# Kernel tuning notes

Measured on AMD Instinct MI355X. Metric: run time of the kernel, lower is better.

## Reference

```python
import jax, jax.numpy as jnp
import numpy as np

EMBED = 1024
HEADS = 16
HEAD_DIM = EMBED // HEADS
B, S = 4, 2048


def setup_inputs() -> dict:
    key = jax.random.key(0)
    ks = jax.random.split(key, 13)
    scale = 1.0 / np.sqrt(EMBED)
    inp = {
        "query": jax.random.normal(ks[0], (B, S, EMBED), dtype=jnp.float32),
        "key": jax.random.normal(ks[1], (B, S, EMBED), dtype=jnp.float32),
        "value": jax.random.normal(ks[2], (B, S, EMBED), dtype=jnp.float32),
        "mask": jax.random.randint(ks[3], (B, 1, S, S), 0, 2) > 0,
        "Wq": jax.random.normal(ks[4], (EMBED, EMBED), dtype=jnp.float32) * scale,
        "bq": jnp.zeros((EMBED,), dtype=jnp.float32),
        "Wk": jax.random.normal(ks[5], (EMBED, EMBED), dtype=jnp.float32) * scale,
        "bk": jnp.zeros((EMBED,), dtype=jnp.float32),
        "Wv": jax.random.normal(ks[6], (EMBED, EMBED), dtype=jnp.float32) * scale,
        "bv": jnp.zeros((EMBED,), dtype=jnp.float32),
        "Wo": jax.random.normal(ks[7], (EMBED, EMBED), dtype=jnp.float32) * scale,
        "bo": jnp.zeros((EMBED,), dtype=jnp.float32),
    }
    return inp


def _split_heads(x):
    b, s, _ = x.shape
    return x.reshape(b, s, HEADS, HEAD_DIM).transpose(0, 2, 1, 3)  # [B,H,S,Dh]


def reference(query, key, value, mask, Wq, bq, Wk, bk, Wv, bv, Wo, bo):
    # Linear projections (torch Linear: x @ W.T + b)
    q = _split_heads(query @ Wq.T + bq)
    k = _split_heads(key @ Wk.T + bk)
    v = _split_heads(value @ Wv.T + bv)
    # scaled dot-product attention with full score matrix (as in source)
    scores = jnp.einsum("bhqd,bhkd->bhqk", q, k) / jnp.sqrt(jnp.float32(HEAD_DIM))
    scores = jnp.where(mask, jnp.float32(-1e9), scores)
    attn = jax.nn.softmax(scores, axis=-1)  # dropout p=0 -> identity
    out = jnp.einsum("bhqk,bhkd->bhqd", attn, v)
    out = out.transpose(0, 2, 1, 3).reshape(out.shape[0], -1, EMBED)
    return out @ Wo.T + bo
```

## Files before the change

kernel.cpp:

```cpp
#include <hip/hip_runtime.h>
#include <cstdint>

#define B_  4
#define H_  16
#define S_  2048
#define DH_ 64
#define E_  1024
#define M_  (B_ * S_)

typedef __attribute__((ext_vector_type(8))) __bf16 bf16x8;
typedef __attribute__((ext_vector_type(4))) __bf16 bf16x4;
typedef __attribute__((ext_vector_type(4))) float  f32x4;

__device__ __forceinline__ uint16_t f2bf(float f) {
    union { float f; uint32_t u; } v; v.f = f;
    uint32_t u = v.u;
    uint32_t r = (u + 0x7fffu + ((u >> 16) & 1u)) >> 16;
    return (uint16_t)r;
}
__device__ __forceinline__ uint32_t pack2(float a, float b) {
    return (uint32_t)f2bf(a) | ((uint32_t)f2bf(b) << 16);
}

__device__ __forceinline__ uint32_t cvt_pk_bf16(float lo, float hi) {
    uint32_t r;
    asm("v_cvt_pk_bf16_f32 %0, %1, %2" : "=v"(r) : "v"(lo), "v"(hi));
    return r;
}

__device__ __forceinline__ float exp2_fast(float x) {
#if __has_builtin(__builtin_amdgcn_exp2f)
    return __builtin_amdgcn_exp2f(x);
#else
    float r; asm("v_exp_f32 %0, %1" : "=v"(r) : "v"(x)); return r;
#endif
}

__device__ __forceinline__ void glds16(const void* g, void* lds_base) {
    __builtin_amdgcn_global_load_lds(
        (const __attribute__((address_space(1))) uint32_t*)g,
        (__attribute__((address_space(3))) uint32_t*)lds_base, 16, 0, 0);
}

__global__ void prep_kernel(const float* __restrict__ q, const float* __restrict__ k,
                            const float* __restrict__ v,
                            const float* __restrict__ w0, const float* __restrict__ w1,
                            const float* __restrict__ w2, const float* __restrict__ w3,
                            uint16_t* __restrict__ wbf,
                            uint16_t* __restrict__ qa, uint16_t* __restrict__ ka,
                            uint16_t* __restrict__ va) {
    int bid = blockIdx.x;
    const float* src; uint16_t* dst; int base;
    if (bid < 2048) {
        int i = bid * 256 + threadIdx.x;
        base = i * 8;
        int wsel = base >> 20;
        src = (wsel == 0) ? w0 : (wsel == 1) ? w1 : (wsel == 2) ? w2 : w3;
        dst = wbf + base;
        base &= 1048575;
    } else {
        int r = bid - 2048;
        int sel = r >> 12;
        int i = (r & 4095) * 256 + threadIdx.x;
        base = i * 8;
        src = (sel == 0) ? q : (sel == 1) ? k : v;
        dst = ((sel == 0) ? qa : (sel == 1) ? ka : va) + base;
    }
    float4 a = *(const float4*)(src + base);
    float4 b = *(const float4*)(src + base + 4);
    uint4 o;
    o.x = pack2(a.x, a.y); o.y = pack2(a.z, a.w);
    o.z = pack2(b.x, b.y); o.w = pack2(b.z, b.w);
    *(uint4*)dst = o;
}

__global__ void mask_bits_kernel(const int* __restrict__ mask, uint64_t* __restrict__ bits) {
    int idx = blockIdx.x * 256 + threadIdx.x;
    uint64_t b = __ballot(mask[idx] != 0);
    if ((threadIdx.x & 63) == 0) bits[idx >> 6] = b;
}

__global__ __launch_bounds__(256, 2)
void gemm_bt_kernel(const uint16_t* __restrict__ A0, const uint16_t* __restrict__ A1,
                    const uint16_t* __restrict__ A2,
                    const uint16_t* __restrict__ Bw0,
                    const float* __restrict__ bias0, const float* __restrict__ bias1,
                    const float* __restrict__ bias2,
                    void* __restrict__ out0, void* __restrict__ out1,
                    void* __restrict__ out2,
                    int multi) {
    const int z = blockIdx.z;
    const uint16_t* A  = (z == 0) ? A0 : (z == 1) ? A1 : A2;
    const uint16_t* Bw = Bw0 + (size_t)z * 1048576;
    const float* bias  = (z == 0) ? bias0 : (z == 1) ? bias1 : bias2;
    void* out          = (z == 0) ? out0 : (z == 1) ? out1 : out2;
    const float scale  = (multi && z == 0) ? 0.18033688f : 1.0f;
    const int mode     = multi ? ((z == 2) ? 2 : 1) : 0;

    const int m0 = blockIdx.y * 128;
    const int n0 = blockIdx.x * 128;

    __shared__ __align__(16) uint16_t As[128 * 64];
    __shared__ __align__(16) uint16_t Bs[128 * 64];

    const int t    = threadIdx.x;
    const int w    = t >> 6;
    const int lane = t & 63;
    const int ln   = lane & 15;
    const int quad = lane >> 4;
    const int wr   = w >> 1;
    const int wc   = w & 1;

    f32x4 acc[4][4];
    const f32x4 z4 = {0.f, 0.f, 0.f, 0.f};
#pragma unroll
    for (int i = 0; i < 4; ++i)
#pragma unroll
        for (int j = 0; j < 4; ++j) acc[i][j] = z4;

    const char* Ag = (const char*)(A  + (size_t)m0 * E_);
    const char* Bg = (const char*)(Bw + (size_t)n0 * E_);
    const int rsub = lane >> 3;
    const int colb = ((lane & 7) ^ rsub) * 16;

    for (int kk = 0; kk < E_; kk += 64) {
#pragma unroll
        for (int c = 0; c < 4; ++c) {
            glds16(Ag + (size_t)(c * 32 + w * 8 + rsub) * 2048 + kk * 2 + colb,
                   (char*)As + c * 4096 + w * 1024);
            glds16(Bg + (size_t)(c * 32 + w * 8 + rsub) * 2048 + kk * 2 + colb,
                   (char*)Bs + c * 4096 + w * 1024);
        }
        __syncthreads();

#pragma unroll
        for (int ks = 0; ks < 2; ++ks) {
            bf16x8 af[4], bf[4];
#pragma unroll
            for (int mt = 0; mt < 4; ++mt)
                af[mt] = *(const bf16x8*)&As[(wr * 64 + mt * 16 + ln) * 64 +
                                             (((ks * 4 + quad) ^ (ln & 7)) * 8)];
#pragma unroll
            for (int nt = 0; nt < 4; ++nt)
                bf[nt] = *(const bf16x8*)&Bs[(wc * 64 + nt * 16 + ln) * 64 +
                                             (((ks * 4 + quad) ^ (ln & 7)) * 8)];
#pragma unroll
            for (int mt = 0; mt < 4; ++mt)
#pragma unroll
                for (int nt = 0; nt < 4; ++nt)
                    acc[mt][nt] = __builtin_amdgcn_mfma_f32_16x16x32_bf16(
                        af[mt], bf[nt], acc[mt][nt], 0, 0, 0);
        }
        __syncthreads();
    }

#pragma unroll
    for (int mt = 0; mt < 4; ++mt) {
        const int rowb = m0 + wr * 64 + mt * 16 + quad * 4;
#pragma unroll
        for (int nt = 0; nt < 4; ++nt) {
            const int col = n0 + wc * 64 + nt * 16 + ln;
            const float bsum = bias[col];
            if (mode == 2) {
                int bb = rowb >> 11, s0 = rowb & 2047, hh = col >> 6, d = col & 63;
                float v0 = acc[mt][nt][0] + bsum, v1 = acc[mt][nt][1] + bsum;
                float v2 = acc[mt][nt][2] + bsum, v3 = acc[mt][nt][3] + bsum;
                uint2 o; o.x = pack2(v0, v1); o.y = pack2(v2, v3);
                *(uint2*)((uint16_t*)out + (((size_t)bb * H_ + hh) * DH_ + d) * S_ + s0) = o;
            } else {
#pragma unroll
                for (int r = 0; r < 4; ++r) {
                    float vv = (acc[mt][nt][r] + bsum) * scale;
                    int rr = rowb + r;
                    if (mode == 1) {
                        int bb = rr >> 11, s = rr & 2047, hh = col >> 6, d = col & 63;
                        ((uint16_t*)out)[(((size_t)bb * H_ + hh) * S_ + s) * DH_ + d] = f2bf(vv);
                    } else {
                        ((float*)out)[(size_t)rr * E_ + col] = vv;
                    }
                }
            }
        }
    }
}

__global__ __launch_bounds__(256, 2)
void attn_kernel(const uint16_t* __restrict__ qb, const uint16_t* __restrict__ kb,
                 const uint16_t* __restrict__ vtb, const uint32_t* __restrict__ mbits,
                 uint16_t* __restrict__ attn_out) {
    const int qt = blockIdx.x;
    const int bh = blockIdx.y;
    const int b  = bh >> 4, h = bh & 15;

    __shared__ __align__(16) char smem[51200];
    uint16_t* k_lds  = (uint16_t*)smem;
    uint16_t* vt_lds = (uint16_t*)(smem + 16384);
    uint16_t* p_all  = (uint16_t*)(smem + 32768);
    uint16_t* q_lds  = p_all;

    const int t    = threadIdx.x;
    const int w    = t >> 6;
    const int lane = t & 63;
    const int ln   = lane & 15;
    const int quad = lane >> 4;
    const int ln2  = ln << 1;

    const char* qg  = (const char*)(qb  + ((size_t)bh * S_ + qt * 64) * DH_);
    const char* kg  = (const char*)(kb  + (size_t)bh * S_ * DH_);
    const char* vtg = (const char*)(vtb + (size_t)bh * DH_ * S_);

    glds16(qg + w * 2048 +    0 + lane * 16, (char*)q_lds + w * 2048);
    glds16(qg + w * 2048 + 1024 + lane * 16, (char*)q_lds + w * 2048 + 1024);
    __syncthreads();

    bf16x8 aq[4][2];
#pragma unroll
    for (int mt = 0; mt < 4; ++mt)
#pragma unroll
        for (int ks = 0; ks < 2; ++ks)
            aq[mt][ks] = *(const bf16x8*)&q_lds[(mt * 16 + ln) * 64 + ks * 32 + quad * 8];

    f32x4 acc_o[4][4];
    const f32x4 z4 = {0.f, 0.f, 0.f, 0.f};
#pragma unroll
    for (int mt = 0; mt < 4; ++mt)
#pragma unroll
        for (int nt = 0; nt < 4; ++nt) acc_o[mt][nt] = z4;
    float lr[4][4];
#pragma unroll
    for (int mt = 0; mt < 4; ++mt)
#pragma unroll
        for (int r = 0; r < 4; ++r) lr[mt][r] = 0.f;

    uint16_t* pw = p_all + w * 2304;
    const uint32_t* mwp = mbits + ((size_t)b * S_ + qt * 64) * (S_ / 32);

    for (int it = 0; it < 16; ++it) {
        const char* kt = kg + it * 16384;
        const int rsub = lane >> 3;
        const int kcol = ((lane & 7) ^ rsub) * 16;
#pragma unroll
        for (int c = 0; c < 4; ++c) {
            const int p    = c * 8 + rsub;
            const int jrow = (p < 16) ? (2 * p) : (2 * p - 31);
            glds16(kt + (size_t)(w * 32 + jrow) * 128 + kcol,
                   (char*)k_lds + w * 4096 + c * 1024);
        }
#pragma unroll
        for (int c = 0; c < 4; ++c) {
            int d0  = w * 16 + c * 4;
            int row = d0 + (lane >> 4);
            int gch = (lane & 15) ^ (row & 15);
            glds16(vtg + (size_t)row * (S_ * 2) + it * 256 + gch * 16,
                   (char*)vt_lds + d0 * 256);
        }
        uint32_t mk[4][4];
#pragma unroll
        for (int mt = 0; mt < 4; ++mt)
#pragma unroll
            for (int r = 0; r < 4; ++r)
                mk[mt][r] = mwp[(size_t)(mt * 16 + quad * 4 + r) * 64 + it * 4 + w];
        __syncthreads();

        f32x4 sc[4][2];
#pragma unroll
        for (int mt = 0; mt < 4; ++mt) { sc[mt][0] = z4; sc[mt][1] = z4; }
#pragma unroll
        for (int ks = 0; ks < 2; ++ks) {
            bf16x8 bk0 = *(const bf16x8*)&k_lds[(w * 32 + ln) * 64 +
                                                (((ks * 4 + quad) ^ (ln & 7)) * 8)];
            bf16x8 bk1 = *(const bf16x8*)&k_lds[(w * 32 + 16 + ln) * 64 +
                                                (((ks * 4 + quad) ^ (ln & 7)) * 8)];
#pragma unroll
            for (int mt = 0; mt < 4; ++mt) {
                sc[mt][0] = __builtin_amdgcn_mfma_f32_16x16x32_bf16(aq[mt][ks], bk0, sc[mt][0], 0, 0, 0);
                sc[mt][1] = __builtin_amdgcn_mfma_f32_16x16x32_bf16(aq[mt][ks], bk1, sc[mt][1], 0, 0, 0);
            }
        }

        bf16x8 bv[4];
#pragma unroll
        for (int nt = 0; nt < 4; ++nt)
            bv[nt] = *(const bf16x8*)&vt_lds[(nt * 16 + ln) * 128 +
                                             (((w * 4 + quad) ^ ln) * 8)];

#pragma unroll
        for (int mt = 0; mt < 4; ++mt)
#pragma unroll
            for (int r = 0; r < 4; ++r) {
                uint32_t sh = mk[mt][r] >> ln2;
                float e0 = (sh & 1u) ? 0.f : exp2_fast(sc[mt][0][r]);
                float e1 = (sh & 2u) ? 0.f : exp2_fast(sc[mt][1][r]);
                lr[mt][r] += e0 + e1;
                *(uint32_t*)&pw[(mt * 16 + quad * 4 + r) * 36 + ln2] = cvt_pk_bf16(e0, e1);
            }

#pragma unroll
        for (int mt = 0; mt < 4; ++mt) {
            bf16x4 lo = *(const bf16x4*)&pw[(mt * 16 + ln) * 36 + quad * 8];
            bf16x4 hi = *(const bf16x4*)&pw[(mt * 16 + ln) * 36 + quad * 8 + 4];
            bf16x8 ap = __builtin_shufflevector(lo, hi, 0, 1, 2, 3, 4, 5, 6, 7);
#pragma unroll
            for (int nt = 0; nt < 4; ++nt)
                acc_o[mt][nt] = __builtin_amdgcn_mfma_f32_16x16x32_bf16(ap, bv[nt], acc_o[mt][nt], 0, 0, 0);
        }
        __syncthreads();
    }

#pragma unroll
    for (int mt = 0; mt < 4; ++mt)
#pragma unroll
        for (int r = 0; r < 4; ++r) {
            float v = lr[mt][r];
            v += __shfl_xor(v, 1);
            v += __shfl_xor(v, 2);
            v += __shfl_xor(v, 4);
            v += __shfl_xor(v, 8);
            lr[mt][r] = v;
        }

    __syncthreads();
    float* obuf = (float*)smem;
    float* lbuf = (float*)(smem + 49920);

    if (ln == 0) {
#pragma unroll
        for (int mt = 0; mt < 4; ++mt)
#pragma unroll
            for (int r = 0; r < 4; ++r)
                lbuf[w * 64 + mt * 16 + quad * 4 + r] = lr[mt][r];
    }
#pragma unroll
    for (int mt = 0; mt < 4; ++mt) {
        if (mt != w) {
            int ridx = mt * 3 + (w > mt ? w - 1 : w);
            float* reg = obuf + ridx * 1040;
#pragma unroll
            for (int nt = 0; nt < 4; ++nt)
#pragma unroll
                for (int rr = 0; rr < 4; ++rr)
                    reg[(quad * 4 + rr) * 65 + nt * 16 + ln] = acc_o[mt][nt][rr];
        }
    }
    __syncthreads();

    f32x4 accf[4];
#pragma unroll
    for (int nt = 0; nt < 4; ++nt) accf[nt] = acc_o[0][nt];
#pragma unroll
    for (int mt = 1; mt < 4; ++mt)
        if (w == mt) {
#pragma unroll
            for (int nt = 0; nt < 4; ++nt) accf[nt] = acc_o[mt][nt];
        }
#pragma unroll
    for (int widx = 0; widx < 3; ++widx) {
        const float* reg = obuf + (w * 3 + widx) * 1040;
#pragma unroll
        for (int nt = 0; nt < 4; ++nt)
#pragma unroll
            for (int rr = 0; rr < 4; ++rr)
                accf[nt][rr] += reg[(quad * 4 + rr) * 65 + nt * 16 + ln];
    }
    float invl[4];
#pragma unroll
    for (int rr = 0; rr < 4; ++rr) {
        int row = w * 16 + quad * 4 + rr;
        float lt = lbuf[row] + lbuf[64 + row] + lbuf[128 + row] + lbuf[192 + row];
        invl[rr] = 1.0f / lt;
    }
    const size_t orow = (size_t)(b * S_ + qt * 64 + w * 16 + quad * 4);
#pragma unroll
    for (int rr = 0; rr < 4; ++rr)
#pragma unroll
        for (int nt = 0; nt < 4; ++nt)
            attn_out[(orow + rr) * E_ + h * 64 + nt * 16 + ln] = f2bf(accf[nt][rr] * invl[rr]);
}

extern "C" void kernel_launch(void* const* d_in, const int* in_sizes, int n_in,
                              void* d_out, int out_size, void* d_ws, size_t ws_size,
                              hipStream_t stream) {
    const float* query = (const float*)d_in[0];
    const float* key_  = (const float*)d_in[1];
    const float* value = (const float*)d_in[2];
    const int*   mask  = (const int*)d_in[3];
    const float* Wq = (const float*)d_in[4];
    const float* bq = (const float*)d_in[5];
    const float* Wk = (const float*)d_in[6];
    const float* bk = (const float*)d_in[7];
    const float* Wv = (const float*)d_in[8];
    const float* bv = (const float*)d_in[9];
    const float* Wo = (const float*)d_in[10];
    const float* bo = (const float*)d_in[11];

    char* ws = (char*)d_ws;
    uint16_t* wbf   = (uint16_t*)ws;
    uint16_t* qa    = (uint16_t*)(ws + (8u   << 20));
    uint16_t* ka    = (uint16_t*)(ws + (24u  << 20));
    uint16_t* va    = (uint16_t*)(ws + (40u  << 20));
    uint16_t* qproj = (uint16_t*)(ws + (56u  << 20));
    uint16_t* kproj = (uint16_t*)(ws + (72u  << 20));
    uint16_t* vtp   = (uint16_t*)(ws + (88u  << 20));
    uint16_t* atto  = (uint16_t*)(ws + (104u << 20));
    uint64_t* mbits = (uint64_t*)(ws + (120u << 20));

    prep_kernel<<<14336, 256, 0, stream>>>(query, key_, value, Wq, Wk, Wv, Wo,
                                           wbf, qa, ka, va);
    mask_bits_kernel<<<65536, 256, 0, stream>>>(mask, mbits);

    gemm_bt_kernel<<<dim3(E_ / 128, M_ / 128, 3), 256, 0, stream>>>(
        qa, ka, va, wbf, bq, bk, bv, qproj, kproj, vtp, 1);

    attn_kernel<<<dim3(S_ / 64, B_ * H_), 256, 0, stream>>>(
        qproj, kproj, vtp, (const uint32_t*)mbits, atto);

    gemm_bt_kernel<<<dim3(E_ / 128, M_ / 128, 1), 256, 0, stream>>>(
        atto, atto, atto, wbf + 3145728, bo, bo, bo, d_out, d_out, d_out, 0);
}
```

Before: 456.6 us.

## Load K/V directly into registers with prefetch and remap blocks per XCD

The attention kernel stops staging Q, K and V^T tiles through LDS. Each lane now loads its MFMA fragments straight from global memory, and the next K tile is prefetched into registers one iteration ahead. This removes the per-iteration __syncthreads barriers and the LDS copies. Separately, the grid is flattened to 1D and blocks are remapped so that all query tiles of one batch-head land on the same XCD, which should improve L2 reuse of K/V. The trade-offs are less-coalesced, cache-dependent global loads, higher register pressure, and a prefetch on the last iteration that reads past the end of the current head's K.

```diff
diff --git a/kernel.cpp b/kernel.cpp
--- a/kernel.cpp
+++ b/kernel.cpp
@@ -188,15 +188,15 @@
 void attn_kernel(const uint16_t* __restrict__ qb, const uint16_t* __restrict__ kb,
                  const uint16_t* __restrict__ vtb, const uint32_t* __restrict__ mbits,
                  uint16_t* __restrict__ attn_out) {
-    const int qt = blockIdx.x;
-    const int bh = blockIdx.y;
-    const int b  = bh >> 4, h = bh & 15;
+    const int wg   = blockIdx.x;
+    const int xcd  = wg & 7;
+    const int rest = wg >> 3;
+    const int qt   = rest & 31;
+    const int bh   = ((rest >> 5) << 3) | xcd;
+    const int b    = bh >> 4, h = bh & 15;
 
     __shared__ __align__(16) char smem[51200];
-    uint16_t* k_lds  = (uint16_t*)smem;
-    uint16_t* vt_lds = (uint16_t*)(smem + 16384);
-    uint16_t* p_all  = (uint16_t*)(smem + 32768);
-    uint16_t* q_lds  = p_all;
+    uint16_t* p_all = (uint16_t*)smem;
 
     const int t    = threadIdx.x;
     const int w    = t >> 6;
@@ -209,16 +209,13 @@
     const char* kg  = (const char*)(kb  + (size_t)bh * S_ * DH_);
     const char* vtg = (const char*)(vtb + (size_t)bh * DH_ * S_);
 
-    glds16(qg + w * 2048 +    0 + lane * 16, (char*)q_lds + w * 2048);
-    glds16(qg + w * 2048 + 1024 + lane * 16, (char*)q_lds + w * 2048 + 1024);
-    __syncthreads();
-
     bf16x8 aq[4][2];
 #pragma unroll
     for (int mt = 0; mt < 4; ++mt)
 #pragma unroll
         for (int ks = 0; ks < 2; ++ks)
-            aq[mt][ks] = *(const bf16x8*)&q_lds[(mt * 16 + ln) * 64 + ks * 32 + quad * 8];
+            aq[mt][ks] = *(const bf16x8*)(qg + (size_t)(mt * 16 + ln) * 128 +
+                                          ks * 64 + quad * 16);
 
     f32x4 acc_o[4][4];
     const f32x4 z4 = {0.f, 0.f, 0.f, 0.f};
@@ -233,56 +230,48 @@
         for (int r = 0; r < 4; ++r) lr[mt][r] = 0.f;
 
     uint16_t* pw = p_all + w * 2304;
-    const uint32_t* mwp = mbits + ((size_t)b * S_ + qt * 64) * (S_ / 32);
+
+    const char* kp0 = kg + (size_t)(w * 32 + ln2) * 128 + quad * 16;
+    const char* kp1 = kg + (size_t)(w * 32 + ln2 + 1) * 128 + quad * 16;
+    const char* vp  = vtg + (size_t)ln * 4096 + w * 64 + quad * 16;
+    const char* mp  = (const char*)(mbits + ((size_t)b * S_ + qt * 64) * 64) +
+                      (quad * 4) * 256 + w * 4;
+
+    bf16x8 kf[2][2];
+#pragma unroll
+    for (int ks = 0; ks < 2; ++ks) {
+        kf[ks][0] = *(const bf16x8*)(kp0 + ks * 64);
+        kf[ks][1] = *(const bf16x8*)(kp1 + ks * 64);
+    }
 
     for (int it = 0; it < 16; ++it) {
-        const char* kt = kg + it * 16384;
-        const int rsub = lane >> 3;
-        const int kcol = ((lane & 7) ^ rsub) * 16;
-#pragma unroll
-        for (int c = 0; c < 4; ++c) {
-            const int p    = c * 8 + rsub;
-            const int jrow = (p < 16) ? (2 * p) : (2 * p - 31);
-            glds16(kt + (size_t)(w * 32 + jrow) * 128 + kcol,
-                   (char*)k_lds + w * 4096 + c * 1024);
-        }
-#pragma unroll
-        for (int c = 0; c < 4; ++c) {
-            int d0  = w * 16 + c * 4;
-            int row = d0 + (lane >> 4);
-            int gch = (lane & 15) ^ (row & 15);
-            glds16(vtg + (size_t)row * (S_ * 2) + it * 256 + gch * 16,
-                   (char*)vt_lds + d0 * 256);
-        }
+        bf16x8 bv[4];
+#pragma unroll
+        for (int nt = 0; nt < 4; ++nt)
+            bv[nt] = *(const bf16x8*)(vp + (size_t)nt * 65536);
         uint32_t mk[4][4];
 #pragma unroll
         for (int mt = 0; mt < 4; ++mt)
 #pragma unroll
             for (int r = 0; r < 4; ++r)
-                mk[mt][r] = mwp[(size_t)(mt * 16 + quad * 4 + r) * 64 + it * 4 + w];
-        __syncthreads();
+                mk[mt][r] = *(const uint32_t*)(mp + mt * 4096 + r * 256);
+        bf16x8 kn[2][2];
+#pragma unroll
+        for (int ks = 0; ks < 2; ++ks) {
+            kn[ks][0] = *(const bf16x8*)(kp0 + 16384 + ks * 64);
+            kn[ks][1] = *(const bf16x8*)(kp1 + 16384 + ks * 64);
+        }
 
         f32x4 sc[4][2];
 #pragma unroll
         for (int mt = 0; mt < 4; ++mt) { sc[mt][0] = z4; sc[mt][1] = z4; }
 #pragma unroll
-        for (int ks = 0; ks < 2; ++ks) {
-            bf16x8 bk0 = *(const bf16x8*)&k_lds[(w * 32 + ln) * 64 +
-                                                (((ks * 4 + quad) ^ (ln & 7)) * 8)];
-            bf16x8 bk1 = *(const bf16x8*)&k_lds[(w * 32 + 16 + ln) * 64 +
-                                                (((ks * 4 + quad) ^ (ln & 7)) * 8)];
+        for (int ks = 0; ks < 2; ++ks)
 #pragma unroll
             for (int mt = 0; mt < 4; ++mt) {
-                sc[mt][0] = __builtin_amdgcn_mfma_f32_16x16x32_bf16(aq[mt][ks], bk0, sc[mt][0], 0, 0, 0);
-                sc[mt][1] = __builtin_amdgcn_mfma_f32_16x16x32_bf16(aq[mt][ks], bk1, sc[mt][1], 0, 0, 0);
+                sc[mt][0] = __builtin_amdgcn_mfma_f32_16x16x32_bf16(aq[mt][ks], kf[ks][0], sc[mt][0], 0, 0, 0);
+                sc[mt][1] = __builtin_amdgcn_mfma_f32_16x16x32_bf16(aq[mt][ks], kf[ks][1], sc[mt][1], 0, 0, 0);
             }
-        }
-
-        bf16x8 bv[4];
-#pragma unroll
-        for (int nt = 0; nt < 4; ++nt)
-            bv[nt] = *(const bf16x8*)&vt_lds[(nt * 16 + ln) * 128 +
-                                             (((w * 4 + quad) ^ ln) * 8)];
 
 #pragma unroll
         for (int mt = 0; mt < 4; ++mt)
@@ -304,7 +293,13 @@
             for (int nt = 0; nt < 4; ++nt)
                 acc_o[mt][nt] = __builtin_amdgcn_mfma_f32_16x16x32_bf16(ap, bv[nt], acc_o[mt][nt], 0, 0, 0);
         }
-        __syncthreads();
+
+#pragma unroll
+        for (int ks = 0; ks < 2; ++ks) {
+            kf[ks][0] = kn[ks][0];
+            kf[ks][1] = kn[ks][1];
+        }
+        kp0 += 16384; kp1 += 16384; vp += 256; mp += 16;
     }
 
 #pragma unroll
@@ -411,7 +406,7 @@
     gemm_bt_kernel<<<dim3(E_ / 128, M_ / 128, 3), 256, 0, stream>>>(
         qa, ka, va, wbf, bq, bk, bv, qproj, kproj, vtp, 1);
 
-    attn_kernel<<<dim3(S_ / 64, B_ * H_), 256, 0, stream>>>(
+    attn_kernel<<<dim3(2048), 256, 0, stream>>>(
         qproj, kproj, vtp, (const uint32_t*)mbits, atto);
 
     gemm_bt_kernel<<<dim3(E_ / 128, M_ / 128, 1), 256, 0, stream>>>(
```

New measurement: 468.9 us. 2.7% more time.

## Split attention by query rows per wave and remap grid for XCD locality

Applied to the files above, without the earlier changes.

The attention kernel now gives each wave 64 query rows over all key chunks. Previously the four waves split the keys of one 64-row tile and combined partial outputs through LDS. This drops the cross-wave reduction and its extra barriers, and each block now covers 256 query rows, so K/V tiles loaded into LDS are reused four times as much. The mask-bit kernel writes the bitmask in a permuted layout so each wave reads its mask words with vector loads. The grid becomes 512 blocks whose index is swizzled so heads stay on the same XCD, at the cost of fewer blocks to fill the GPU and more registers per wave.

```diff
diff --git a/kernel.cpp b/kernel.cpp
--- a/kernel.cpp
+++ b/kernel.cpp
@@ -74,10 +74,27 @@
     *(uint4*)dst = o;
 }
 
-__global__ void mask_bits_kernel(const int* __restrict__ mask, uint64_t* __restrict__ bits) {
+__global__ void mask_bits_kernel(const int* __restrict__ mask, uint32_t* __restrict__ bits) {
     int idx = blockIdx.x * 256 + threadIdx.x;
-    uint64_t b = __ballot(mask[idx] != 0);
-    if ((threadIdx.x & 63) == 0) bits[idx >> 6] = b;
+    uint64_t bl = __ballot(mask[idx] != 0);
+    if ((threadIdx.x & 63) == 0) {
+        int col  = idx & 2047;
+        int row  = (idx >> 11) & 2047;
+        int b    = idx >> 22;
+        int qt8  = row >> 8;
+        int rw   = row & 255;
+        int w    = rw >> 6, sl = rw & 63;
+        int mt   = sl >> 4, quad = (sl >> 2) & 3, r = sl & 3;
+        int c0   = col >> 5;
+#pragma unroll
+        for (int half = 0; half < 2; ++half) {
+            int c  = c0 + half;
+            int it = c >> 2, js = c & 3;
+            size_t i = (((((((size_t)(b * 8 + qt8) * 4 + w) * 4 + js) * 16 + it)
+                          * 4 + quad) * 4 + mt) * 4 + r);
+            bits[i] = (uint32_t)(half ? (bl >> 32) : bl);
+        }
+    }
 }
 
 __global__ __launch_bounds__(256, 2)
@@ -188,15 +205,17 @@
 void attn_kernel(const uint16_t* __restrict__ qb, const uint16_t* __restrict__ kb,
                  const uint16_t* __restrict__ vtb, const uint32_t* __restrict__ mbits,
                  uint16_t* __restrict__ attn_out) {
-    const int qt = blockIdx.x;
-    const int bh = blockIdx.y;
-    const int b  = bh >> 4, h = bh & 15;
+    const int wg   = blockIdx.x;
+    const int xcd  = wg & 7;
+    const int rest = wg >> 3;
+    const int qt8  = rest & 7;
+    const int bh   = ((rest >> 3) << 3) | xcd;
+    const int b    = bh >> 4, h = bh & 15;
 
     __shared__ __align__(16) char smem[51200];
     uint16_t* k_lds  = (uint16_t*)smem;
     uint16_t* vt_lds = (uint16_t*)(smem + 16384);
     uint16_t* p_all  = (uint16_t*)(smem + 32768);
-    uint16_t* q_lds  = p_all;
 
     const int t    = threadIdx.x;
     const int w    = t >> 6;
@@ -205,20 +224,17 @@
     const int quad = lane >> 4;
     const int ln2  = ln << 1;
 
-    const char* qg  = (const char*)(qb  + ((size_t)bh * S_ + qt * 64) * DH_);
+    const char* qg  = (const char*)(qb  + ((size_t)bh * S_ + qt8 * 256) * DH_);
     const char* kg  = (const char*)(kb  + (size_t)bh * S_ * DH_);
     const char* vtg = (const char*)(vtb + (size_t)bh * DH_ * S_);
 
-    glds16(qg + w * 2048 +    0 + lane * 16, (char*)q_lds + w * 2048);
-    glds16(qg + w * 2048 + 1024 + lane * 16, (char*)q_lds + w * 2048 + 1024);
-    __syncthreads();
-
     bf16x8 aq[4][2];
 #pragma unroll
     for (int mt = 0; mt < 4; ++mt)
 #pragma unroll
         for (int ks = 0; ks < 2; ++ks)
-            aq[mt][ks] = *(const bf16x8*)&q_lds[(mt * 16 + ln) * 64 + ks * 32 + quad * 8];
+            aq[mt][ks] = *(const bf16x8*)(qg + (size_t)(w * 64 + mt * 16 + ln) * 128 +
+                                          ks * 64 + quad * 16);
 
     f32x4 acc_o[4][4];
     const f32x4 z4 = {0.f, 0.f, 0.f, 0.f};
@@ -233,12 +249,13 @@
         for (int r = 0; r < 4; ++r) lr[mt][r] = 0.f;
 
     uint16_t* pw = p_all + w * 2304;
-    const uint32_t* mwp = mbits + ((size_t)b * S_ + qt * 64) * (S_ / 32);
+    const uint32_t* mw = mbits + (size_t)(b * 8 + qt8) * 16384 + w * 4096 + quad * 16;
+
+    const int rsub = lane >> 3;
+    const int kcol = ((lane & 7) ^ rsub) * 16;
 
     for (int it = 0; it < 16; ++it) {
-        const char* kt = kg + it * 16384;
-        const int rsub = lane >> 3;
-        const int kcol = ((lane & 7) ^ rsub) * 16;
+        const char* kt = kg + (size_t)it * 16384;
 #pragma unroll
         for (int c = 0; c < 4; ++c) {
             const int p    = c * 8 + rsub;
@@ -254,59 +271,63 @@
             glds16(vtg + (size_t)row * (S_ * 2) + it * 256 + gch * 16,
                    (char*)vt_lds + d0 * 256);
         }
-        uint32_t mk[4][4];
-#pragma unroll
-        for (int mt = 0; mt < 4; ++mt)
-#pragma unroll
-            for (int r = 0; r < 4; ++r)
-                mk[mt][r] = mwp[(size_t)(mt * 16 + quad * 4 + r) * 64 + it * 4 + w];
         __syncthreads();
 
-        f32x4 sc[4][2];
-#pragma unroll
-        for (int mt = 0; mt < 4; ++mt) { sc[mt][0] = z4; sc[mt][1] = z4; }
-#pragma unroll
-        for (int ks = 0; ks < 2; ++ks) {
-            bf16x8 bk0 = *(const bf16x8*)&k_lds[(w * 32 + ln) * 64 +
-                                                (((ks * 4 + quad) ^ (ln & 7)) * 8)];
-            bf16x8 bk1 = *(const bf16x8*)&k_lds[(w * 32 + 16 + ln) * 64 +
-                                                (((ks * 4 + quad) ^ (ln & 7)) * 8)];
+#pragma unroll
+        for (int js = 0; js < 4; ++js) {
+            uint4 mk4[4];
+#pragma unroll
+            for (int mt = 0; mt < 4; ++mt)
+                mk4[mt] = *(const uint4*)(mw + js * 1024 + it * 64 + mt * 4);
+            bf16x8 bv[4];
+#pragma unroll
+            for (int nt = 0; nt < 4; ++nt)
+                bv[nt] = *(const bf16x8*)&vt_lds[(nt * 16 + ln) * 128 +
+                                                 (((js * 4 + quad) ^ ln) * 8)];
+
+            f32x4 sc[4][2];
+#pragma unroll
+            for (int mt = 0; mt < 4; ++mt) { sc[mt][0] = z4; sc[mt][1] = z4; }
+#pragma unroll
+            for (int ks = 0; ks < 2; ++ks) {
+                bf16x8 bk0 = *(const bf16x8*)&k_lds[(js * 32 + ln) * 64 +
+                                                    (((ks * 4 + quad) ^ (ln & 7)) * 8)];
+                bf16x8 bk1 = *(const bf16x8*)&k_lds[(js * 32 + 16 + ln) * 64 +
+                                                    (((ks * 4 + quad) ^ (ln & 7)) * 8)];
+#pragma unroll
+                for (int mt = 0; mt < 4; ++mt) {
+                    sc[mt][0] = __builtin_amdgcn_mfma_f32_16x16x32_bf16(aq[mt][ks], bk0, sc[mt][0], 0, 0, 0);
+                    sc[mt][1] = __builtin_amdgcn_mfma_f32_16x16x32_bf16(aq[mt][ks], bk1, sc[mt][1], 0, 0, 0);
+                }
+            }
+
 #pragma unroll
             for (int mt = 0; mt < 4; ++mt) {
-                sc[mt][0] = __builtin_amdgcn_mfma_f32_16x16x32_bf16(aq[mt][ks], bk0, sc[mt][0], 0, 0, 0);
-                sc[mt][1] = __builtin_amdgcn_mfma_f32_16x16x32_bf16(aq[mt][ks], bk1, sc[mt][1], 0, 0, 0);
+                const uint32_t* mkp = (const uint32_t*)&mk4[mt];
+#pragma unroll
+                for (int r = 0; r < 4; ++r) {
+                    uint32_t sh = mkp[r] >> ln2;
+                    float e0 = (sh & 1u) ? 0.f : exp2_fast(sc[mt][0][r]);
+                    float e1 = (sh & 2u) ? 0.f : exp2_fast(sc[mt][1][r]);
+                    lr[mt][r] += e0 + e1;
+                    *(uint32_t*)&pw[(mt * 16 + quad * 4 + r) * 36 + ln2] = cvt_pk_bf16(e0, e1);
+                }
             }
-        }
-
-        bf16x8 bv[4];
-#pragma unroll
-        for (int nt = 0; nt < 4; ++nt)
-            bv[nt] = *(const bf16x8*)&vt_lds[(nt * 16 + ln) * 128 +
-                                             (((w * 4 + quad) ^ ln) * 8)];
-
-#pragma unroll
-        for (int mt = 0; mt < 4; ++mt)
-#pragma unroll
-            for (int r = 0; r < 4; ++r) {
-                uint32_t sh = mk[mt][r] >> ln2;
-                float e0 = (sh & 1u) ? 0.f : exp2_fast(sc[mt][0][r]);
-                float e1 = (sh & 2u) ? 0.f : exp2_fast(sc[mt][1][r]);
-                lr[mt][r] += e0 + e1;
-                *(uint32_t*)&pw[(mt * 16 + quad * 4 + r) * 36 + ln2] = cvt_pk_bf16(e0, e1);
+
+#pragma unroll
+            for (int mt = 0; mt < 4; ++mt) {
+                bf16x4 lo = *(const bf16x4*)&pw[(mt * 16 + ln) * 36 + quad * 8];
+                bf16x4 hi = *(const bf16x4*)&pw[(mt * 16 + ln) * 36 + quad * 8 + 4];
+                bf16x8 ap = __builtin_shufflevector(lo, hi, 0, 1, 2, 3, 4, 5, 6, 7);
+#pragma unroll
+                for (int nt = 0; nt < 4; ++nt)
+                    acc_o[mt][nt] = __builtin_amdgcn_mfma_f32_16x16x32_bf16(ap, bv[nt], acc_o[mt][nt], 0, 0, 0);
             }
-
-#pragma unroll
-        for (int mt = 0; mt < 4; ++mt) {
-            bf16x4 lo = *(const bf16x4*)&pw[(mt * 16 + ln) * 36 + quad * 8];
-            bf16x4 hi = *(const bf16x4*)&pw[(mt * 16 + ln) * 36 + quad * 8 + 4];
-            bf16x8 ap = __builtin_shufflevector(lo, hi, 0, 1, 2, 3, 4, 5, 6, 7);
-#pragma unroll
-            for (int nt = 0; nt < 4; ++nt)
-                acc_o[mt][nt] = __builtin_amdgcn_mfma_f32_16x16x32_bf16(ap, bv[nt], acc_o[mt][nt], 0, 0, 0);
         }
         __syncthreads();
     }
 
+    float invl[4][4];
 #pragma unroll
     for (int mt = 0; mt < 4; ++mt)
 #pragma unroll
@@ -316,65 +337,20 @@
             v += __shfl_xor(v, 2);
             v += __shfl_xor(v, 4);
             v += __shfl_xor(v, 8);
-            lr[mt][r] = v;
-        }
-
-    __syncthreads();
-    float* obuf = (float*)smem;
-    float* lbuf = (float*)(smem + 49920);
-
-    if (ln == 0) {
-#pragma unroll
-        for (int mt = 0; mt < 4; ++mt)
-#pragma unroll
-            for (int r = 0; r < 4; ++r)
-                lbuf[w * 64 + mt * 16 + quad * 4 + r] = lr[mt][r];
-    }
-#pragma unroll
-    for (int mt = 0; mt < 4; ++mt) {
-        if (mt != w) {
-            int ridx = mt * 3 + (w > mt ? w - 1 : w);
-            float* reg = obuf + ridx * 1040;
+            invl[mt][r] = 1.0f / v;
+        }
+
+    const size_t orow0 = (size_t)b * S_ + qt8 * 256 + w * 64;
+#pragma unroll
+    for (int mt = 0; mt < 4; ++mt)
+#pragma unroll
+        for (int r = 0; r < 4; ++r) {
+            const size_t row = orow0 + mt * 16 + quad * 4 + r;
 #pragma unroll
             for (int nt = 0; nt < 4; ++nt)
-#pragma unroll
-                for (int rr = 0; rr < 4; ++rr)
-                    reg[(quad * 4 + rr) * 65 + nt * 16 + ln] = acc_o[mt][nt][rr];
-        }
-    }
-    __syncthreads();
-
-    f32x4 accf[4];
-#pragma unroll
-    for (int nt = 0; nt < 4; ++nt) accf[nt] = acc_o[0][nt];
-#pragma unroll
-    for (int mt = 1; mt < 4; ++mt)
-        if (w == mt) {
-#pragma unroll
-            for (int nt = 0; nt < 4; ++nt) accf[nt] = acc_o[mt][nt];
-        }
-#pragma unroll
-    for (int widx = 0; widx < 3; ++widx) {
-        const float* reg = obuf + (w * 3 + widx) * 1040;
-#pragma unroll
-        for (int nt = 0; nt < 4; ++nt)
-#pragma unroll
-            for (int rr = 0; rr < 4; ++rr)
-                accf[nt][rr] += reg[(quad * 4 + rr) * 65 + nt * 16 + ln];
-    }
-    float invl[4];
-#pragma unroll
-    for (int rr = 0; rr < 4; ++rr) {
-        int row = w * 16 + quad * 4 + rr;
-        float lt = lbuf[row] + lbuf[64 + row] + lbuf[128 + row] + lbuf[192 + row];
-        invl[rr] = 1.0f / lt;
-    }
-    const size_t orow = (size_t)(b * S_ + qt * 64 + w * 16 + quad * 4);
-#pragma unroll
-    for (int rr = 0; rr < 4; ++rr)
-#pragma unroll
-        for (int nt = 0; nt < 4; ++nt)
-            attn_out[(orow + rr) * E_ + h * 64 + nt * 16 + ln] = f2bf(accf[nt][rr] * invl[rr]);
+                attn_out[row * E_ + h * 64 + nt * 16 + ln] =
+                    f2bf(acc_o[mt][nt][r] * invl[mt][r]);
+        }
 }
 
 extern "C" void kernel_launch(void* const* d_in, const int* in_sizes, int n_in,
@@ -402,7 +378,7 @@
     uint16_t* kproj = (uint16_t*)(ws + (72u  << 20));
     uint16_t* vtp   = (uint16_t*)(ws + (88u  << 20));
     uint16_t* atto  = (uint16_t*)(ws + (104u << 20));
-    uint64_t* mbits = (uint64_t*)(ws + (120u << 20));
+    uint32_t* mbits = (uint32_t*)(ws + (120u << 20));
 
     prep_kernel<<<14336, 256, 0, stream>>>(query, key_, value, Wq, Wk, Wv, Wo,
                                            wbf, qa, ka, va);
@@ -411,8 +387,8 @@
     gemm_bt_kernel<<<dim3(E_ / 128, M_ / 128, 3), 256, 0, stream>>>(
         qa, ka, va, wbf, bq, bk, bv, qproj, kproj, vtp, 1);
 
-    attn_kernel<<<dim3(S_ / 64, B_ * H_), 256, 0, stream>>>(
-        qproj, kproj, vtp, (const uint32_t*)mbits, atto);
+    attn_kernel<<<dim3(512), 256, 0, stream>>>(
+        qproj, kproj, vtp, mbits, atto);
 
     gemm_bt_kernel<<<dim3(E_ / 128, M_ / 128, 1), 256, 0, stream>>>(
         atto, atto, atto, wbf + 3145728, bo, bo, bo, d_out, d_out, d_out, 0);
```

New measurement: 429.6 us. -5.9%, faster.
